# Optimization experiments

Hardware: AMD Instinct MI355X
Metric: run time of the kernel (lower is better)

Reference implementation:

```python
import jax, jax.numpy as jnp
import numpy as np

WS = 8        # window size
NUM_HEADS = 4 # attention heads


def setup_inputs() -> dict:
    key = jax.random.key(0)
    k1, k2, k3 = jax.random.split(key, 3)
    B, N, C = 32, 4096, 128
    x = jax.random.normal(k1, (B, N, C), dtype=jnp.float32)
    w_qkv = jax.random.normal(k2, (3 * C, C), dtype=jnp.float32) * (C ** -0.5)
    w_proj = jax.random.normal(k3, (C, C), dtype=jnp.float32) * (C ** -0.5)
    b_proj = jnp.zeros((C,), dtype=jnp.float32)
    return {"x": x, "w_qkv": w_qkv, "w_proj": w_proj, "b_proj": b_proj, "H": 64, "W": 64}


def reference(x, w_qkv, w_proj, b_proj, H, W):
    B, N, C = x.shape
    ws, nh = WS, NUM_HEADS
    hd = C // nh
    scale = hd ** -0.5
    hg, wg = H // ws, W // ws
    G = hg * wg          # total windows
    S = ws * ws          # tokens per window
    # partition into windows: [B, hg, ws, wg, ws, C] -> [B, G, S, C]
    xg = x.reshape(B, hg, ws, wg, ws, C).transpose(0, 1, 3, 2, 4, 5).reshape(B, G, S, C)
    # qkv projection (no bias)
    qkv = jnp.einsum('bgsc,oc->bgso', xg, w_qkv)
    qkv = qkv.reshape(B, G, S, 3, nh, hd).transpose(3, 0, 1, 4, 2, 5)  # [3,B,G,nh,S,hd]
    q, k, v = qkv[0], qkv[1], qkv[2]
    attn = jnp.einsum('bgnsd,bgntd->bgnst', q, k) * scale
    attn = jax.nn.softmax(attn, axis=-1)
    out = jnp.einsum('bgnst,bgntd->bgnsd', attn, v)
    # [B,G,nh,S,hd] -> [B,G,S,C] -> un-window -> [B,N,C]
    out = out.transpose(0, 1, 3, 2, 4).reshape(B, hg, wg, ws, ws, C)
    out = out.transpose(0, 1, 3, 2, 4, 5).reshape(B, N, C)
    return jnp.einsum('bnc,oc->bno', out, w_proj) + b_proj
```

## Files before the change

### kernel.cpp

```cpp
#include <hip/hip_runtime.h>
#include <cstdint>

typedef short short8 __attribute__((ext_vector_type(8)));
typedef float floatx4 __attribute__((ext_vector_type(4)));
typedef unsigned short ushortx4 __attribute__((ext_vector_type(4)));

__device__ __forceinline__ unsigned short f2bf(float f) {
  union { float f; unsigned u; } v; v.f = f;
  unsigned r = v.u + 0x7FFFu + ((v.u >> 16) & 1u);
  return (unsigned short)(r >> 16);
}
__device__ __forceinline__ float bf2f(unsigned short h) {
  union { unsigned u; float f; } v; v.u = ((unsigned)h) << 16; return v.f;
}

#define MFMA16B(A, B, C) __builtin_amdgcn_mfma_f32_16x16x32_bf16((A), (B), (C), 0, 0, 0)
#define LDS_FENCE() asm volatile("" ::: "memory")

__global__ void __launch_bounds__(256) prep_weights(const float* __restrict__ wq,
                                                    const float* __restrict__ wp,
                                                    unsigned short* __restrict__ wq_h,
                                                    unsigned short* __restrict__ wp_h) {
  int i = blockIdx.x * 256 + threadIdx.x;
  if (i < 384 * 128) wq_h[i] = f2bf(wq[i]);
  if (i < 128 * 128) wp_h[i] = f2bf(wp[i]);
}

__global__ void __launch_bounds__(256, 3) win_attn(const float* __restrict__ x,
                                                   const unsigned short* __restrict__ wqh,
                                                   const unsigned short* __restrict__ wph,
                                                   const float* __restrict__ bias,
                                                   float* __restrict__ out) {
  __shared__ char smem[49152];

  const int tid = threadIdx.x;
  const int wv = tid >> 6;
  const int lane = tid & 63;
  const int lr = lane & 15;
  const int lg = lane >> 4;
  const int swz = (lr & 7) << 4;

  const int bid = blockIdx.x;
  const int b = bid >> 6;
  const int g = bid & 63;
  const int gh = g >> 3, gw = g & 7;
  const size_t base = (size_t)b * (4096 * 128);

  char* regA = smem + wv * 8192;
  char* regV = smem + 32768 + wv * 4096;
  char* osb  = smem;

  const float SCALE = 0.17677669529663687f;

#pragma unroll
  for (int mt = 0; mt < 4; ++mt) {
    const int s = mt * 16 + lr;
    const int n = gh * 512 + (s >> 3) * 64 + gw * 8 + (s & 7);
    const float* xp = x + base + (size_t)n * 128 + lg * 8;
    short8 ah[4], al[4];
#pragma unroll
    for (int ks = 0; ks < 4; ++ks) {
      float4 u = *(const float4*)(xp + ks * 32);
      float4 w = *(const float4*)(xp + ks * 32 + 4);
      float f[8] = {u.x, u.y, u.z, u.w, w.x, w.y, w.z, w.w};
      short8 hh, ll;
#pragma unroll
      for (int j = 0; j < 8; ++j) {
        unsigned short hb = f2bf(f[j]);
        hh[j] = (short)hb;
        ll[j] = (short)f2bf(f[j] - bf2f(hb));
      }
      ah[ks] = hh;
      al[ks] = ll;
    }
#pragma unroll
    for (int m = 0; m < 3; ++m) {
#pragma unroll
      for (int jt = 0; jt < 2; ++jt) {
        floatx4 acc = {0.f, 0.f, 0.f, 0.f};
        const unsigned short* wb =
            wqh + (size_t)(m * 128 + wv * 32 + jt * 16 + lr) * 128 + lg * 8;
#pragma unroll
        for (int ks = 0; ks < 4; ++ks) {
          short8 bw = *(const short8*)(wb + ks * 32);
          acc = MFMA16B(ah[ks], bw, acc);
          acc = MFMA16B(al[ks], bw, acc);
        }
        if (m == 2) {
          ushortx4 vv;
#pragma unroll
          for (int r = 0; r < 4; ++r) vv[r] = f2bf(acc[r]);
          const int d = jt * 16 + lr;
          *(ushortx4*)(regV + ((d * 128 + mt * 32 + lg * 8) ^ swz)) = vv;
        } else {
#pragma unroll
          for (int r = 0; r < 4; ++r) {
            const int s0 = mt * 16 + 4 * lg + r;
            const int col = (m ? 32 : 0) + jt * 16 + lr;
            const float v = (m == 0) ? acc[r] * SCALE : acc[r];
            *(unsigned short*)(regA + ((s0 * 128 + col * 2) ^ ((s0 & 7) << 4))) =
                f2bf(v);
          }
        }
      }
    }
  }

  LDS_FENCE();

  short8 kf[4], qf[4];
#pragma unroll
  for (int i = 0; i < 4; ++i) {
    const int row = i * 16 + lr;
    qf[i] = *(const short8*)(regA + ((row * 128 + 16 * lg) ^ swz));
    kf[i] = *(const short8*)(regA + ((row * 128 + 64 + 16 * lg) ^ swz));
  }
  floatx4 sc[4][4];
#pragma unroll
  for (int mt = 0; mt < 4; ++mt)
#pragma unroll
    for (int nt = 0; nt < 4; ++nt) {
      floatx4 z = {0.f, 0.f, 0.f, 0.f};
      sc[mt][nt] = MFMA16B(kf[mt], qf[nt], z);
    }

  float mx[4], inv[4];
#pragma unroll
  for (int nt = 0; nt < 4; ++nt) {
    float m0 = -1e30f;
#pragma unroll
    for (int mt = 0; mt < 4; ++mt)
#pragma unroll
      for (int r = 0; r < 4; ++r) m0 = fmaxf(m0, sc[mt][nt][r]);
    m0 = fmaxf(m0, __shfl_xor(m0, 16));
    m0 = fmaxf(m0, __shfl_xor(m0, 32));
    mx[nt] = m0;
  }
#pragma unroll
  for (int nt = 0; nt < 4; ++nt) {
    float s0 = 0.f;
#pragma unroll
    for (int mt = 0; mt < 4; ++mt)
#pragma unroll
      for (int r = 0; r < 4; ++r) {
        float e = __expf(sc[mt][nt][r] - mx[nt]);
        sc[mt][nt][r] = e;
        s0 += e;
      }
    s0 += __shfl_xor(s0, 16);
    s0 += __shfl_xor(s0, 32);
    inv[nt] = 1.f / s0;
  }

#pragma unroll
  for (int nt = 0; nt < 4; ++nt) {
    const int row = nt * 16 + lr;
#pragma unroll
    for (int mt = 0; mt < 4; ++mt) {
      ushortx4 pv;
#pragma unroll
      for (int r = 0; r < 4; ++r) pv[r] = f2bf(sc[mt][nt][r] * inv[nt]);
      *(ushortx4*)(regA + ((row * 128 + mt * 32 + lg * 8) ^ swz)) = pv;
    }
  }

  LDS_FENCE();

  short8 vf[2][2], pf[4][2];
#pragma unroll
  for (int dt = 0; dt < 2; ++dt)
#pragma unroll
    for (int ks = 0; ks < 2; ++ks)
      vf[dt][ks] = *(const short8*)(regV + (((16 * dt + lr) * 128 + ks * 64 + 16 * lg) ^ swz));
#pragma unroll
  for (int st = 0; st < 4; ++st)
#pragma unroll
    for (int ks = 0; ks < 2; ++ks)
      pf[st][ks] = *(const short8*)(regA + (((16 * st + lr) * 128 + ks * 64 + 16 * lg) ^ swz));
  floatx4 ot[2][4];
#pragma unroll
  for (int dt = 0; dt < 2; ++dt)
#pragma unroll
    for (int st = 0; st < 4; ++st) {
      floatx4 z = {0.f, 0.f, 0.f, 0.f};
      ot[dt][st] = z;
#pragma unroll
      for (int ks = 0; ks < 2; ++ks)
        ot[dt][st] = MFMA16B(vf[dt][ks], pf[st][ks], ot[dt][st]);
    }

  __syncthreads();

#pragma unroll
  for (int st = 0; st < 4; ++st)
#pragma unroll
    for (int dt = 0; dt < 2; ++dt) {
      ushortx4 ov;
#pragma unroll
      for (int r = 0; r < 4; ++r) ov[r] = f2bf(ot[dt][st][r]);
      *(ushortx4*)(osb + (16 * st + lr) * 272 + (wv * 32 + dt * 16 + 4 * lg) * 2) = ov;
    }

  __syncthreads();

  short8 ao[4];
#pragma unroll
  for (int ks = 0; ks < 4; ++ks)
    ao[ks] = *(const short8*)(osb + (16 * wv + lr) * 272 + ks * 64 + 16 * lg);
#pragma unroll
  for (int nt = 0; nt < 8; ++nt) {
    floatx4 acc = {0.f, 0.f, 0.f, 0.f};
    const unsigned short* wb = wph + (size_t)(nt * 16 + lr) * 128 + lg * 8;
#pragma unroll
    for (int ks = 0; ks < 4; ++ks)
      acc = MFMA16B(ao[ks], *(const short8*)(wb + ks * 32), acc);
    const float bb = bias[nt * 16 + lr];
#pragma unroll
    for (int r = 0; r < 4; ++r) {
      const int s0 = 16 * wv + 4 * lg + r;
      const int n = gh * 512 + (s0 >> 3) * 64 + gw * 8 + (s0 & 7);
      out[base + (size_t)n * 128 + nt * 16 + lr] = acc[r] + bb;
    }
  }
}

extern "C" void kernel_launch(void* const* d_in, const int* in_sizes, int n_in,
                              void* d_out, int out_size, void* d_ws, size_t ws_size,
                              hipStream_t stream) {
  (void)in_sizes; (void)n_in; (void)out_size; (void)ws_size;
  const float* x  = (const float*)d_in[0];
  const float* wq = (const float*)d_in[1];
  const float* wp = (const float*)d_in[2];
  const float* bp = (const float*)d_in[3];
  float* out = (float*)d_out;
  unsigned short* wq_h = (unsigned short*)d_ws;
  unsigned short* wp_h = wq_h + 384 * 128;
  prep_weights<<<192, 256, 0, stream>>>(wq, wp, wq_h, wp_h);
  win_attn<<<2048, 256, 0, stream>>>(x, wq_h, wp_h, bp, out);
}
```

Before: 249.1 us.

## Stage split-bf16 input tile in LDS and load QKV weights once per wave

The 64x128 fp32 window tile is now loaded cooperatively with coalesced reads, split into hi/lo bf16 parts, and staged in LDS behind a barrier. Each wave then loads its QKV weight fragments once and reuses them across all four row tiles, instead of reloading them from global memory per row tile. The Q/K/V fragments are held in registers and written to a new per-wave LDS layout after a second barrier. Scalar bf16 rounding is replaced by the packed bf162 conversion intrinsic. The cost is two extra block barriers, LDS reads of the A operands, and a larger live register set.

```diff
diff --git a/kernel.cpp b/kernel.cpp
--- a/kernel.cpp
+++ b/kernel.cpp
@@ -1,21 +1,34 @@
 #include <hip/hip_runtime.h>
+#include <hip/hip_bf16.h>
 #include <cstdint>
 
 typedef short short8 __attribute__((ext_vector_type(8)));
 typedef float floatx4 __attribute__((ext_vector_type(4)));
 typedef unsigned short ushortx4 __attribute__((ext_vector_type(4)));
+typedef unsigned int uintx4 __attribute__((ext_vector_type(4)));
+
+#define MFMA16B(A, B, C) __builtin_amdgcn_mfma_f32_16x16x32_bf16((A), (B), (C), 0, 0, 0)
+#define LDS_FENCE() asm volatile("" ::: "memory")
 
 __device__ __forceinline__ unsigned short f2bf(float f) {
   union { float f; unsigned u; } v; v.f = f;
   unsigned r = v.u + 0x7FFFu + ((v.u >> 16) & 1u);
   return (unsigned short)(r >> 16);
 }
-__device__ __forceinline__ float bf2f(unsigned short h) {
-  union { unsigned u; float f; } v; v.u = ((unsigned)h) << 16; return v.f;
-}
-
-#define MFMA16B(A, B, C) __builtin_amdgcn_mfma_f32_16x16x32_bf16((A), (B), (C), 0, 0, 0)
-#define LDS_FENCE() asm volatile("" ::: "memory")
+__device__ __forceinline__ unsigned pack_bf2(float a, float b) {
+  __hip_bfloat162 h = __float22bfloat162_rn(float2{a, b});
+  union { __hip_bfloat162 h; unsigned u; } c; c.h = h; return c.u;
+}
+__device__ __forceinline__ float lo_half_f(unsigned u) {
+  union { unsigned u; float f; } c; c.u = u << 16; return c.f;
+}
+__device__ __forceinline__ float hi_half_f(unsigned u) {
+  union { unsigned u; float f; } c; c.u = u & 0xffff0000u; return c.f;
+}
+__device__ __forceinline__ ushortx4 pack_bf4(float a, float b, float c, float d) {
+  uint2 p; p.x = pack_bf2(a, b); p.y = pack_bf2(c, d);
+  union { uint2 u; ushortx4 s; } v; v.u = p; return v.s;
+}
 
 __global__ void __launch_bounds__(256) prep_weights(const float* __restrict__ wq,
                                                     const float* __restrict__ wp,
@@ -32,88 +45,91 @@
                                                    const float* __restrict__ bias,
                                                    float* __restrict__ out) {
   __shared__ char smem[49152];
-
   const int tid = threadIdx.x;
-  const int wv = tid >> 6;
-  const int lane = tid & 63;
-  const int lr = lane & 15;
-  const int lg = lane >> 4;
-  const int swz = (lr & 7) << 4;
-
+  const int wv = tid >> 6, lane = tid & 63, lr = lane & 15, lg = lane >> 4;
   const int bid = blockIdx.x;
-  const int b = bid >> 6;
-  const int g = bid & 63;
-  const int gh = g >> 3, gw = g & 7;
+  const int b = bid >> 6, g = bid & 63, gh = g >> 3, gw = g & 7;
   const size_t base = (size_t)b * (4096 * 128);
 
-  char* regA = smem + wv * 8192;
-  char* regV = smem + 32768 + wv * 4096;
-  char* osb  = smem;
-
+  {
+    const int r = tid >> 2, c0 = (tid & 3) * 32;
+    const int n = gh * 512 + (r >> 3) * 64 + gw * 8 + (r & 7);
+    const float4* xp = (const float4*)(x + base + (size_t)n * 128 + c0);
+    const int rb = r * 512, sz = (r & 7) << 4;
+#pragma unroll
+    for (int i = 0; i < 4; ++i) {
+      float4 u = xp[2 * i], w = xp[2 * i + 1];
+      unsigned h0 = pack_bf2(u.x, u.y), h1 = pack_bf2(u.z, u.w);
+      unsigned h2 = pack_bf2(w.x, w.y), h3 = pack_bf2(w.z, w.w);
+      unsigned l0 = pack_bf2(u.x - lo_half_f(h0), u.y - hi_half_f(h0));
+      unsigned l1 = pack_bf2(u.z - lo_half_f(h1), u.w - hi_half_f(h1));
+      unsigned l2 = pack_bf2(w.x - lo_half_f(h2), w.y - hi_half_f(h2));
+      unsigned l3 = pack_bf2(w.z - lo_half_f(h3), w.w - hi_half_f(h3));
+      uintx4 hv = {h0, h1, h2, h3}, lv = {l0, l1, l2, l3};
+      *(uintx4*)(smem + ((rb + (c0 + 8 * i) * 2) ^ sz)) = hv;
+      *(uintx4*)(smem + ((rb + 256 + (c0 + 8 * i) * 2) ^ sz)) = lv;
+    }
+  }
+  __syncthreads();
+
+  const int swzx = (lr & 7) << 4;
   const float SCALE = 0.17677669529663687f;
 
-#pragma unroll
-  for (int mt = 0; mt < 4; ++mt) {
-    const int s = mt * 16 + lr;
-    const int n = gh * 512 + (s >> 3) * 64 + gw * 8 + (s & 7);
-    const float* xp = x + base + (size_t)n * 128 + lg * 8;
-    short8 ah[4], al[4];
-#pragma unroll
-    for (int ks = 0; ks < 4; ++ks) {
-      float4 u = *(const float4*)(xp + ks * 32);
-      float4 w = *(const float4*)(xp + ks * 32 + 4);
-      float f[8] = {u.x, u.y, u.z, u.w, w.x, w.y, w.z, w.w};
-      short8 hh, ll;
-#pragma unroll
-      for (int j = 0; j < 8; ++j) {
-        unsigned short hb = f2bf(f[j]);
-        hh[j] = (short)hb;
-        ll[j] = (short)f2bf(f[j] - bf2f(hb));
+  ushortx4 pk[6][4];
+#pragma unroll
+  for (int j = 0; j < 6; ++j) {
+    const int m = j >> 1, jt = j & 1;
+    const unsigned short* wb = wqh + (size_t)(m * 128 + wv * 32 + jt * 16 + lr) * 128 + lg * 8;
+    short8 bw[4];
+    bw[0] = *(const short8*)(wb);
+    bw[1] = *(const short8*)(wb + 32);
+    bw[2] = *(const short8*)(wb + 64);
+    bw[3] = *(const short8*)(wb + 96);
+    const float fs = (j < 2) ? SCALE : 1.0f;
+#pragma unroll
+    for (int mt = 0; mt < 4; ++mt) {
+      const int rbase = (16 * mt + lr) * 512 + lg * 16;
+      floatx4 acc = {0.f, 0.f, 0.f, 0.f};
+#pragma unroll
+      for (int kk = 0; kk < 8; ++kk) {
+        short8 a = *(const short8*)(smem + ((rbase + kk * 64) ^ swzx));
+        acc = MFMA16B(a, bw[kk & 3], acc);
       }
-      ah[ks] = hh;
-      al[ks] = ll;
-    }
-#pragma unroll
-    for (int m = 0; m < 3; ++m) {
-#pragma unroll
-      for (int jt = 0; jt < 2; ++jt) {
-        floatx4 acc = {0.f, 0.f, 0.f, 0.f};
-        const unsigned short* wb =
-            wqh + (size_t)(m * 128 + wv * 32 + jt * 16 + lr) * 128 + lg * 8;
-#pragma unroll
-        for (int ks = 0; ks < 4; ++ks) {
-          short8 bw = *(const short8*)(wb + ks * 32);
-          acc = MFMA16B(ah[ks], bw, acc);
-          acc = MFMA16B(al[ks], bw, acc);
-        }
-        if (m == 2) {
-          ushortx4 vv;
-#pragma unroll
-          for (int r = 0; r < 4; ++r) vv[r] = f2bf(acc[r]);
-          const int d = jt * 16 + lr;
-          *(ushortx4*)(regV + ((d * 128 + mt * 32 + lg * 8) ^ swz)) = vv;
-        } else {
-#pragma unroll
-          for (int r = 0; r < 4; ++r) {
-            const int s0 = mt * 16 + 4 * lg + r;
-            const int col = (m ? 32 : 0) + jt * 16 + lr;
-            const float v = (m == 0) ? acc[r] * SCALE : acc[r];
-            *(unsigned short*)(regA + ((s0 * 128 + col * 2) ^ ((s0 & 7) << 4))) =
-                f2bf(v);
-          }
-        }
+      pk[j][mt] = pack_bf4(acc[0] * fs, acc[1] * fs, acc[2] * fs, acc[3] * fs);
+    }
+  }
+  __syncthreads();
+
+  char* const wbase = smem + wv * 12288;
+#pragma unroll
+  for (int j = 0; j < 4; ++j) {
+    char* qk = wbase + (j >> 1) * 4096;
+    const int d = (j & 1) * 16 + lr;
+#pragma unroll
+    for (int mt = 0; mt < 4; ++mt)
+#pragma unroll
+      for (int r = 0; r < 4; ++r) {
+        const int s = 16 * mt + 4 * lg + r;
+        *(unsigned short*)(qk + ((s * 64 + d * 2) ^ ((s & 3) << 4))) = pk[j][mt][r];
       }
-    }
-  }
-
+  }
+#pragma unroll
+  for (int jt = 0; jt < 2; ++jt) {
+    const int d = jt * 16 + lr;
+#pragma unroll
+    for (int mt = 0; mt < 4; ++mt)
+      *(ushortx4*)(wbase + 8192 + ((d * 128 + (16 * mt + 4 * lg) * 2) ^ ((d & 7) << 4))) =
+          pk[4 + jt][mt];
+  }
   LDS_FENCE();
 
-  short8 kf[4], qf[4];
+  const int swzq = (lr & 3) << 4, swzp = (lr & 7) << 4;
+  short8 ka[4], qb[4];
 #pragma unroll
   for (int i = 0; i < 4; ++i) {
-    const int row = i * 16 + lr;
-    qf[i] = *(const short8*)(regA + ((row * 128 + 16 * lg) ^ swz));
-    kf[i] = *(const short8*)(regA + ((row * 128 + 64 + 16 * lg) ^ swz));
+    const int ro = (16 * i + lr) * 64 + lg * 16;
+    qb[i] = *(const short8*)(wbase + (ro ^ swzq));
+    ka[i] = *(const short8*)(wbase + 4096 + (ro ^ swzq));
   }
   floatx4 sc[4][4];
 #pragma unroll
@@ -121,10 +137,10 @@
 #pragma unroll
     for (int nt = 0; nt < 4; ++nt) {
       floatx4 z = {0.f, 0.f, 0.f, 0.f};
-      sc[mt][nt] = MFMA16B(kf[mt], qf[nt], z);
-    }
-
-  float mx[4], inv[4];
+      sc[mt][nt] = MFMA16B(ka[mt], qb[nt], z);
+    }
+
+  float inv[4];
 #pragma unroll
   for (int nt = 0; nt < 4; ++nt) {
     float m0 = -1e30f;
@@ -134,16 +150,12 @@
       for (int r = 0; r < 4; ++r) m0 = fmaxf(m0, sc[mt][nt][r]);
     m0 = fmaxf(m0, __shfl_xor(m0, 16));
     m0 = fmaxf(m0, __shfl_xor(m0, 32));
-    mx[nt] = m0;
-  }
-#pragma unroll
-  for (int nt = 0; nt < 4; ++nt) {
     float s0 = 0.f;
 #pragma unroll
     for (int mt = 0; mt < 4; ++mt)
 #pragma unroll
       for (int r = 0; r < 4; ++r) {
-        float e = __expf(sc[mt][nt][r] - mx[nt]);
+        float e = __expf(sc[mt][nt][r] - m0);
         sc[mt][nt][r] = e;
         s0 += e;
       }
@@ -154,39 +166,36 @@
 
 #pragma unroll
   for (int nt = 0; nt < 4; ++nt) {
-    const int row = nt * 16 + lr;
-#pragma unroll
-    for (int mt = 0; mt < 4; ++mt) {
-      ushortx4 pv;
-#pragma unroll
-      for (int r = 0; r < 4; ++r) pv[r] = f2bf(sc[mt][nt][r] * inv[nt]);
-      *(ushortx4*)(regA + ((row * 128 + mt * 32 + lg * 8) ^ swz)) = pv;
-    }
-  }
-
+    const int rb = (16 * nt + lr) * 128;
+#pragma unroll
+    for (int mt = 0; mt < 4; ++mt)
+      *(ushortx4*)(wbase + ((rb + (16 * mt + 4 * lg) * 2) ^ swzp)) =
+          pack_bf4(sc[mt][nt][0] * inv[nt], sc[mt][nt][1] * inv[nt],
+                   sc[mt][nt][2] * inv[nt], sc[mt][nt][3] * inv[nt]);
+  }
   LDS_FENCE();
 
-  short8 vf[2][2], pf[4][2];
+  short8 va[2][2], pb[4][2];
 #pragma unroll
   for (int dt = 0; dt < 2; ++dt)
 #pragma unroll
     for (int ks = 0; ks < 2; ++ks)
-      vf[dt][ks] = *(const short8*)(regV + (((16 * dt + lr) * 128 + ks * 64 + 16 * lg) ^ swz));
+      va[dt][ks] = *(const short8*)(wbase + 8192 +
+                   (((16 * dt + lr) * 128 + ks * 64 + lg * 16) ^ swzp));
 #pragma unroll
   for (int st = 0; st < 4; ++st)
 #pragma unroll
     for (int ks = 0; ks < 2; ++ks)
-      pf[st][ks] = *(const short8*)(regA + (((16 * st + lr) * 128 + ks * 64 + 16 * lg) ^ swz));
+      pb[st][ks] = *(const short8*)(wbase +
+                   (((16 * st + lr) * 128 + ks * 64 + lg * 16) ^ swzp));
   floatx4 ot[2][4];
 #pragma unroll
   for (int dt = 0; dt < 2; ++dt)
 #pragma unroll
     for (int st = 0; st < 4; ++st) {
       floatx4 z = {0.f, 0.f, 0.f, 0.f};
-      ot[dt][st] = z;
-#pragma unroll
-      for (int ks = 0; ks < 2; ++ks)
-        ot[dt][st] = MFMA16B(vf[dt][ks], pf[st][ks], ot[dt][st]);
+      z = MFMA16B(va[dt][0], pb[st][0], z);
+      ot[dt][st] = MFMA16B(va[dt][1], pb[st][1], z);
     }
 
   __syncthreads();
@@ -194,26 +203,23 @@
 #pragma unroll
   for (int st = 0; st < 4; ++st)
 #pragma unroll
-    for (int dt = 0; dt < 2; ++dt) {
-      ushortx4 ov;
-#pragma unroll
-      for (int r = 0; r < 4; ++r) ov[r] = f2bf(ot[dt][st][r]);
-      *(ushortx4*)(osb + (16 * st + lr) * 272 + (wv * 32 + dt * 16 + 4 * lg) * 2) = ov;
-    }
-
+    for (int dt = 0; dt < 2; ++dt)
+      *(ushortx4*)(smem + (16 * st + lr) * 272 + (wv * 32 + dt * 16 + 4 * lg) * 2) =
+          pack_bf4(ot[dt][st][0], ot[dt][st][1], ot[dt][st][2], ot[dt][st][3]);
   __syncthreads();
 
   short8 ao[4];
 #pragma unroll
-  for (int ks = 0; ks < 4; ++ks)
-    ao[ks] = *(const short8*)(osb + (16 * wv + lr) * 272 + ks * 64 + 16 * lg);
+  for (int kk = 0; kk < 4; ++kk)
+    ao[kk] = *(const short8*)(smem + (16 * wv + lr) * 272 + kk * 64 + lg * 16);
 #pragma unroll
   for (int nt = 0; nt < 8; ++nt) {
+    const unsigned short* wb = wph + (size_t)(nt * 16 + lr) * 128 + lg * 8;
     floatx4 acc = {0.f, 0.f, 0.f, 0.f};
-    const unsigned short* wb = wph + (size_t)(nt * 16 + lr) * 128 + lg * 8;
-#pragma unroll
-    for (int ks = 0; ks < 4; ++ks)
-      acc = MFMA16B(ao[ks], *(const short8*)(wb + ks * 32), acc);
+    acc = MFMA16B(ao[0], *(const short8*)(wb), acc);
+    acc = MFMA16B(ao[1], *(const short8*)(wb + 32), acc);
+    acc = MFMA16B(ao[2], *(const short8*)(wb + 64), acc);
+    acc = MFMA16B(ao[3], *(const short8*)(wb + 96), acc);
     const float bb = bias[nt * 16 + lr];
 #pragma unroll
     for (int r = 0; r < 4; ++r) {
```

After: 223.4 us. -10.3%, faster.
